# Kernel optimization log

Hardware: AMD Instinct MI355X
Metric: run time of the kernel (lower is better)

## Reference

```python
import jax, jax.numpy as jnp
import numpy as np

SMOOTH = 1.0

def setup_inputs() -> dict:
    key = jax.random.key(0)
    k1, k2 = jax.random.split(key)
    shape = (2, 4, 64, 256, 256)  # [B, organs, D, H, W]
    predict = jax.random.normal(k1, shape, dtype=jnp.float32)
    target = jax.random.uniform(k2, shape, dtype=jnp.float32)
    return {"predict": predict, "target": target}

def reference(predict, target):
    # sigmoid over whole prediction tensor (done once in DiceLoss.forward)
    p = jax.nn.sigmoid(predict)
    B, O, D = p.shape[0], p.shape[1], p.shape[2]
    # BinaryDiceLoss views each [D, H, W] organ slice as (D, H*W):
    pf = p.reshape(B, O, D, -1)
    tf = target.reshape(B, O, D, -1)
    num = jnp.sum(pf * tf, axis=-1)                      # [B, O, D]
    den = jnp.sum(pf, axis=-1) + jnp.sum(tf, axis=-1) + SMOOTH
    dice_loss = 1.0 - 2.0 * num / den                    # [B, O, D]
    # slices with first element == -1 are ignored
    valid = (tf[..., 0] != -1).astype(dice_loss.dtype)   # [B, O, D]
    per_slice_avg = jnp.sum(dice_loss * valid, axis=-1) / jnp.sum(valid, axis=-1)  # [B, O]
    # outer loop averages over all B*4 (b, organ) pairs
    return jnp.mean(per_slice_avg)
```

## Files before the change

### kernel.cpp

```cpp
#include <hip/hip_runtime.h>


constexpr int HW       = 256 * 256;
constexpr int NSLICE   = 2 * 4 * 64;
constexpr int NPAIR    = 2 * 4;
constexpr int CHUNKS   = 4;
constexpr int NBLOCK   = NSLICE * CHUNKS;
constexpr int THREADS  = 256;
constexpr int CHUNK_F4 = HW / 4 / CHUNKS;
constexpr int ITERS    = CHUNK_F4 / THREADS;
constexpr int BATCH    = 8;
constexpr int OUTER    = ITERS / BATCH;


__global__ __launch_bounds__(THREADS, 2) void dice_stage1(
    const float* __restrict__ predict,
    const float* __restrict__ target,
    float* __restrict__ ws)
{
    const int blk = blockIdx.x;
    const int tid = threadIdx.x;
    const size_t base4 = (size_t)blk * CHUNK_F4;
    const float4* __restrict__ p4 = (const float4*)predict + base4;
    const float4* __restrict__ t4 = (const float4*)target  + base4;

    float s_pt0 = 0.f, s_pt1 = 0.f, s_p0 = 0.f, s_p1 = 0.f, s_t0 = 0.f, s_t1 = 0.f;

    for (int it = 0; it < OUTER; ++it) {
        float4 pv[BATCH], tv[BATCH];
#pragma unroll
        for (int j = 0; j < BATCH; ++j)
            pv[j] = p4[(it * BATCH + j) * THREADS + tid];
#pragma unroll
        for (int j = 0; j < BATCH; ++j)
            tv[j] = t4[(it * BATCH + j) * THREADS + tid];
        __builtin_amdgcn_sched_barrier(0);
#pragma unroll
        for (int j = 0; j < BATCH; ++j) {
            float e0 = 1.f / (1.f + __expf(-pv[j].x));
            float e1 = 1.f / (1.f + __expf(-pv[j].y));
            float e2 = 1.f / (1.f + __expf(-pv[j].z));
            float e3 = 1.f / (1.f + __expf(-pv[j].w));
            s_pt0 += e0 * tv[j].x + e1 * tv[j].y;
            s_pt1 += e2 * tv[j].z + e3 * tv[j].w;
            s_p0  += e0 + e1;
            s_p1  += e2 + e3;
            s_t0  += tv[j].x + tv[j].y;
            s_t1  += tv[j].z + tv[j].w;
        }
    }

    float s_pt = s_pt0 + s_pt1;
    float s_p  = s_p0 + s_p1;
    float s_t  = s_t0 + s_t1;

#pragma unroll
    for (int off = 32; off > 0; off >>= 1) {
        s_pt += __shfl_down(s_pt, off, 64);
        s_p  += __shfl_down(s_p,  off, 64);
        s_t  += __shfl_down(s_t,  off, 64);
    }

    __shared__ float l_pt[THREADS / 64];
    __shared__ float l_p [THREADS / 64];
    __shared__ float l_t [THREADS / 64];
    const int wave = tid >> 6;
    const int lane = tid & 63;
    if (lane == 0) { l_pt[wave] = s_pt; l_p[wave] = s_p; l_t[wave] = s_t; }
    __syncthreads();

    if (tid == 0) {
        float pt = 0.f, sp = 0.f, st = 0.f;
#pragma unroll
        for (int w = 0; w < THREADS / 64; ++w) {
            pt += l_pt[w]; sp += l_p[w]; st += l_t[w];
        }
        ws[blk]              = pt;
        ws[NBLOCK + blk]     = sp;
        ws[2 * NBLOCK + blk] = st;
    }
}

__global__ __launch_bounds__(NSLICE) void dice_stage2(
    const float* __restrict__ ws,
    const float* __restrict__ target,
    float* __restrict__ out)
{
    const int tid = threadIdx.x;
    float pt = 0.f, sp = 0.f, st = 0.f;
#pragma unroll
    for (int c = 0; c < CHUNKS; ++c) {
        const int i = tid * CHUNKS + c;
        pt += ws[i];
        sp += ws[NBLOCK + i];
        st += ws[2 * NBLOCK + i];
    }
    const float valid = (target[(size_t)tid * HW] != -1.0f) ? 1.0f : 0.0f;
    const float den   = sp + st + 1.0f;
    const float dice  = 1.0f - 2.0f * pt / den;

    float dv = dice * valid;
    float v  = valid;
#pragma unroll
    for (int off = 32; off > 0; off >>= 1) {
        dv += __shfl_down(dv, off, 64);
        v  += __shfl_down(v,  off, 64);
    }
    __shared__ float pair_avg[NPAIR];
    const int wave = tid >> 6;
    const int lane = tid & 63;
    if (lane == 0) pair_avg[wave] = dv / v;
    __syncthreads();
    if (tid == 0) {
        float s = 0.f;
#pragma unroll
        for (int w = 0; w < NPAIR; ++w) s += pair_avg[w];
        out[0] = s * (1.0f / NPAIR);
    }
}

extern "C" void kernel_launch(void* const* d_in, const int* in_sizes, int n_in,
                              void* d_out, int out_size, void* d_ws, size_t ws_size,
                              hipStream_t stream) {
    const float* predict = (const float*)d_in[0];
    const float* target  = (const float*)d_in[1];
    float* ws  = (float*)d_ws;
    float* out = (float*)d_out;

    dice_stage1<<<NBLOCK, THREADS, 0, stream>>>(predict, target, ws);
    dice_stage2<<<1, NSLICE, 0, stream>>>(ws, target, out);
}
```

Measured before the change: 278.3 us.

## Switch to grid-strided persistent blocks with per-step atomic slice accumulation

Stage 1 now runs a fixed grid of 2048 blocks. Each block strides across the whole tensor one float4 per thread per step, does a full block reduction every step, and atomically adds the partial sums into per-slice accumulators. A separate kernel zeroes the accumulators first, and predict is read with nontemporal loads. The aim is better load balance and less cache pollution. In exchange it adds a __syncthreads and atomics on every step, drops the batched loads that gave memory-level parallelism, and adds one more kernel launch.

New measurement: 284.6 us. +2.3%, slower.

```diff
diff --git a/kernel.cpp b/kernel.cpp
--- a/kernel.cpp
+++ b/kernel.cpp
@@ -1,83 +1,83 @@
 #include <hip/hip_runtime.h>
 
 
-constexpr int HW       = 256 * 256;
-constexpr int NSLICE   = 2 * 4 * 64;
-constexpr int NPAIR    = 2 * 4;
-constexpr int CHUNKS   = 4;
-constexpr int NBLOCK   = NSLICE * CHUNKS;
-constexpr int THREADS  = 256;
-constexpr int CHUNK_F4 = HW / 4 / CHUNKS;
-constexpr int ITERS    = CHUNK_F4 / THREADS;
-constexpr int BATCH    = 8;
-constexpr int OUTER    = ITERS / BATCH;
+constexpr int HW        = 256 * 256;
+constexpr int NSLICE    = 2 * 4 * 64;
+constexpr int NPAIR     = 2 * 4;
+constexpr int THREADS   = 256;
+constexpr int NBLK      = 2048;
+constexpr int F4_SLICE  = HW / 4;
+constexpr int F4_TOTAL  = NSLICE * F4_SLICE;
+constexpr int F4_STEP   = NBLK * THREADS;
+constexpr int KSTEPS    = F4_TOTAL / F4_STEP;
+constexpr int SLICES_PER_STEP = F4_STEP / F4_SLICE;
+constexpr int BLK_PER_SLICE   = F4_SLICE / THREADS;
+
+typedef float v4 __attribute__((ext_vector_type(4)));
 
 
-__global__ __launch_bounds__(THREADS, 2) void dice_stage1(
+__global__ void zero_ws(float* __restrict__ ws)
+{
+    const int i = blockIdx.x * blockDim.x + threadIdx.x;
+    if (i < 3 * NSLICE) ws[i] = 0.f;
+}
+
+__global__ __launch_bounds__(THREADS) void dice_stage1(
     const float* __restrict__ predict,
     const float* __restrict__ target,
     float* __restrict__ ws)
 {
-    const int blk = blockIdx.x;
-    const int tid = threadIdx.x;
-    const size_t base4 = (size_t)blk * CHUNK_F4;
-    const float4* __restrict__ p4 = (const float4*)predict + base4;
-    const float4* __restrict__ t4 = (const float4*)target  + base4;
+    const int b    = blockIdx.x;
+    const int tid  = threadIdx.x;
+    const int wave = tid >> 6;
+    const int lane = tid & 63;
+    const int slice_base = b / BLK_PER_SLICE;
 
-    float s_pt0 = 0.f, s_pt1 = 0.f, s_p0 = 0.f, s_p1 = 0.f, s_t0 = 0.f, s_t1 = 0.f;
+    __shared__ float l_pt[2][THREADS / 64];
+    __shared__ float l_p [2][THREADS / 64];
+    __shared__ float l_t [2][THREADS / 64];
 
-    for (int it = 0; it < OUTER; ++it) {
-        float4 pv[BATCH], tv[BATCH];
-#pragma unroll
-        for (int j = 0; j < BATCH; ++j)
-            pv[j] = p4[(it * BATCH + j) * THREADS + tid];
-#pragma unroll
-        for (int j = 0; j < BATCH; ++j)
-            tv[j] = t4[(it * BATCH + j) * THREADS + tid];
-        __builtin_amdgcn_sched_barrier(0);
-#pragma unroll
-        for (int j = 0; j < BATCH; ++j) {
-            float e0 = 1.f / (1.f + __expf(-pv[j].x));
-            float e1 = 1.f / (1.f + __expf(-pv[j].y));
-            float e2 = 1.f / (1.f + __expf(-pv[j].z));
-            float e3 = 1.f / (1.f + __expf(-pv[j].w));
-            s_pt0 += e0 * tv[j].x + e1 * tv[j].y;
-            s_pt1 += e2 * tv[j].z + e3 * tv[j].w;
-            s_p0  += e0 + e1;
-            s_p1  += e2 + e3;
-            s_t0  += tv[j].x + tv[j].y;
-            s_t1  += tv[j].z + tv[j].w;
-        }
-    }
+    const v4* __restrict__ p4 = (const v4*)predict;
+    const v4* __restrict__ t4 = (const v4*)target;
 
-    float s_pt = s_pt0 + s_pt1;
-    float s_p  = s_p0 + s_p1;
-    float s_t  = s_t0 + s_t1;
+    for (int k = 0; k < KSTEPS; ++k) {
+        const size_t g = (size_t)k * F4_STEP + (size_t)b * THREADS + tid;
+        const v4 pv = __builtin_nontemporal_load(p4 + g);
+        const v4 tv = t4[g];
+
+        const float e0 = 1.f / (1.f + __expf(-pv.x));
+        const float e1 = 1.f / (1.f + __expf(-pv.y));
+        const float e2 = 1.f / (1.f + __expf(-pv.z));
+        const float e3 = 1.f / (1.f + __expf(-pv.w));
+
+        float s_pt = e0 * tv.x + e1 * tv.y + e2 * tv.z + e3 * tv.w;
+        float s_p  = (e0 + e1) + (e2 + e3);
+        float s_t  = (tv.x + tv.y) + (tv.z + tv.w);
 
 #pragma unroll
-    for (int off = 32; off > 0; off >>= 1) {
-        s_pt += __shfl_down(s_pt, off, 64);
-        s_p  += __shfl_down(s_p,  off, 64);
-        s_t  += __shfl_down(s_t,  off, 64);
-    }
-
-    __shared__ float l_pt[THREADS / 64];
-    __shared__ float l_p [THREADS / 64];
-    __shared__ float l_t [THREADS / 64];
-    const int wave = tid >> 6;
-    const int lane = tid & 63;
-    if (lane == 0) { l_pt[wave] = s_pt; l_p[wave] = s_p; l_t[wave] = s_t; }
-    __syncthreads();
-
-    if (tid == 0) {
-        float pt = 0.f, sp = 0.f, st = 0.f;
+        for (int off = 32; off > 0; off >>= 1) {
+            s_pt += __shfl_down(s_pt, off, 64);
+            s_p  += __shfl_down(s_p,  off, 64);
+            s_t  += __shfl_down(s_t,  off, 64);
+        }
+        const int par = k & 1;
+        if (lane == 0) {
+            l_pt[par][wave] = s_pt;
+            l_p [par][wave] = s_p;
+            l_t [par][wave] = s_t;
+        }
+        __syncthreads();
+        if (tid == 0) {
+            float pt = 0.f, sp = 0.f, st = 0.f;
 #pragma unroll
-        for (int w = 0; w < THREADS / 64; ++w) {
-            pt += l_pt[w]; sp += l_p[w]; st += l_t[w];
+            for (int w = 0; w < THREADS / 64; ++w) {
+                pt += l_pt[par][w]; sp += l_p[par][w]; st += l_t[par][w];
+            }
+            const int s = k * SLICES_PER_STEP + slice_base;
+            atomicAdd(&ws[s],              pt);
+            atomicAdd(&ws[NSLICE + s],     sp);
+            atomicAdd(&ws[2 * NSLICE + s], st);
         }
-        ws[blk]              = pt;
-        ws[NBLOCK + blk]     = sp;
-        ws[2 * NBLOCK + blk] = st;
     }
 }
 
@@ -87,14 +87,10 @@
     float* __restrict__ out)
 {
     const int tid = threadIdx.x;
-    float pt = 0.f, sp = 0.f, st = 0.f;
-#pragma unroll
-    for (int c = 0; c < CHUNKS; ++c) {
-        const int i = tid * CHUNKS + c;
-        pt += ws[i];
-        sp += ws[NBLOCK + i];
-        st += ws[2 * NBLOCK + i];
-    }
+    const float pt = ws[tid];
+    const float sp = ws[NSLICE + tid];
+    const float st = ws[2 * NSLICE + tid];
+
     const float valid = (target[(size_t)tid * HW] != -1.0f) ? 1.0f : 0.0f;
     const float den   = sp + st + 1.0f;
     const float dice  = 1.0f - 2.0f * pt / den;
@@ -127,6 +123,7 @@
     float* ws  = (float*)d_ws;
     float* out = (float*)d_out;
 
-    dice_stage1<<<NBLOCK, THREADS, 0, stream>>>(predict, target, ws);
+    zero_ws<<<3, 512, 0, stream>>>(ws);
+    dice_stage1<<<NBLK, THREADS, 0, stream>>>(predict, target, ws);
     dice_stage2<<<1, NSLICE, 0, stream>>>(ws, target, out);
 }
```
